# Optimization experiments

Hardware: AMD Instinct MI355X
Metric: run time of the kernel (lower is better)

The kernel has to match this reference:

```python
import jax, jax.numpy as jnp
import numpy as np

COMMITMENT_COST = 0.25  # pg_nn.VectorQuantizer default


def setup_inputs() -> dict:
    key = jax.random.key(0)
    k1, k2, k3, k4 = jax.random.split(key, 4)
    B, C, H, W = 32, 128, 64, 64
    D, K = 64, 512
    x = jax.random.normal(k1, (B, C, H, W), jnp.float32)
    # 1x1 conv == per-pixel linear projection; store weight as [D, C]
    conv_w = jax.random.normal(k2, (D, C), jnp.float32) * (1.0 / np.sqrt(C))
    conv_b = jax.random.normal(k3, (D,), jnp.float32) * 0.01
    # VectorQuantizer init: uniform(-1/K, 1/K)
    codebook = jax.random.uniform(k4, (K, D), jnp.float32, -1.0 / K, 1.0 / K)
    return {"x": x, "conv_w": conv_w, "conv_b": conv_b, "codebook": codebook}


def reference(x, conv_w, conv_b, codebook):
    # 1x1 conv projection: [B,C,H,W] -> [B,D,H,W]
    z = jnp.einsum('bchw,dc->bdhw', x, conv_w) + conv_b[None, :, None, None]
    B, D, H, W = z.shape
    flat = z.transpose(0, 2, 3, 1).reshape(-1, D)  # [B*H*W, D]
    # squared L2 distances to each codebook vector: [B*H*W, K]
    dists = (jnp.sum(flat * flat, axis=1, keepdims=True)
             - 2.0 * flat @ codebook.T
             + jnp.sum(codebook * codebook, axis=1))
    idx = jnp.argmin(dists, axis=1)  # [B*H*W]
    quantized = codebook[idx].reshape(B, H, W, D).transpose(0, 3, 1, 2)
    # VQ losses (commitment + embedding)
    commitment = COMMITMENT_COST * jnp.mean(jnp.square(jax.lax.stop_gradient(quantized) - z))
    emb_loss = jnp.mean(jnp.square(quantized - jax.lax.stop_gradient(z)))
    loss = commitment + emb_loss
    # straight-through estimator
    quantized_st = z + jax.lax.stop_gradient(quantized - z)
    return quantized_st, loss
```

## Files before the change

### kernel.cpp

```cpp
#include <hip/hip_runtime.h>
#include <hip/hip_bf16.h>
#include <math.h>

#define CIN   128
#define DDIM  64
#define KCB   512
#define HWSZ  4096
#define NPIX  131072
#define NOUTQ 8388608
#define XPAD  136

typedef short bf16x8 __attribute__((ext_vector_type(8)));
typedef float f32x4  __attribute__((ext_vector_type(4)));
typedef unsigned int u32x2 __attribute__((ext_vector_type(2)));

__device__ __forceinline__ unsigned int bcu(float f){ union{float f;unsigned int u;}v; v.f=f; return v.u; }
__device__ __forceinline__ float bcf(unsigned int u){ union{unsigned int u;float f;}v; v.u=u; return v.f; }
__device__ __forceinline__ unsigned int pkbf(float a, float b){
    union { __hip_bfloat162 h; unsigned int u; } v;
    v.h = __float22bfloat162_rn(make_float2(a, b));
    return v.u;
}

#define MFMA16(A, B, C) __builtin_amdgcn_mfma_f32_16x16x32_bf16((A), (B), (C), 0, 0, 0)

__device__ __forceinline__ void proj_tile(
    const float (&xr)[32], unsigned short* xrow,
    const unsigned short* sWA, const float* sBias,
    int lg, int klg, int l,
    f32x4& zA, f32x4& zB, f32x4& zC, f32x4& zD, bf16x8& zb0, bf16x8& zb1)
{
    #pragma unroll
    for (int j = 0; j < 8; ++j) {
        u32x2 pv = { pkbf(xr[4*j+0], xr[4*j+1]), pkbf(xr[4*j+2], xr[4*j+3]) };
        *(u32x2*)(xrow + lg * 32 + 4 * j) = pv;
    }
    zA = *(const f32x4*)(sBias +  0 + klg);
    zB = *(const f32x4*)(sBias + 16 + klg);
    zC = *(const f32x4*)(sBias + 32 + klg);
    zD = *(const f32x4*)(sBias + 48 + klg);
    #pragma unroll
    for (int ks = 0; ks < 4; ++ks) {
        bf16x8 xf = *(const bf16x8*)(xrow + ks * 32 + lg * 8);
        bf16x8 w0 = *(const bf16x8*)(sWA + ((0 * 4 + ks) * 64 + l) * 8);
        bf16x8 w1 = *(const bf16x8*)(sWA + ((1 * 4 + ks) * 64 + l) * 8);
        bf16x8 w2 = *(const bf16x8*)(sWA + ((2 * 4 + ks) * 64 + l) * 8);
        bf16x8 w3 = *(const bf16x8*)(sWA + ((3 * 4 + ks) * 64 + l) * 8);
        zA = MFMA16(w0, xf, zA);
        zB = MFMA16(w1, xf, zB);
        zC = MFMA16(w2, xf, zC);
        zD = MFMA16(w3, xf, zD);
    }
    unsigned int* zr = (unsigned int*)xrow;
    u32x2 z0 = { pkbf(zA[0], zA[1]), pkbf(zA[2], zA[3]) };
    u32x2 z1 = { pkbf(zB[0], zB[1]), pkbf(zB[2], zB[3]) };
    u32x2 z2 = { pkbf(zC[0], zC[1]), pkbf(zC[2], zC[3]) };
    u32x2 z3 = { pkbf(zD[0], zD[1]), pkbf(zD[2], zD[3]) };
    *(u32x2*)(zr +  0 + lg * 2) = z0;
    *(u32x2*)(zr +  8 + lg * 2) = z1;
    *(u32x2*)(zr + 16 + lg * 2) = z2;
    *(u32x2*)(zr + 24 + lg * 2) = z3;
    zb0 = *(const bf16x8*)(xrow + lg * 8);
    zb1 = *(const bf16x8*)(xrow + 32 + lg * 8);
}

__global__ __launch_bounds__(1024, 4) void vq_mfma(
    const float* __restrict__ x,
    const float* __restrict__ w,
    const float* __restrict__ bias,
    const float* __restrict__ cb,
    float* __restrict__ out,
    float* __restrict__ part)
{
    __shared__ __align__(16) unsigned short sCbA[KCB * DDIM];
    __shared__ __align__(16) unsigned short sWA[DDIM * CIN];
    __shared__ __align__(16) float sCbn[KCB];
    __shared__ __align__(16) float sBias[DDIM];
    __shared__ __align__(16) unsigned short sX[16 * 16 * XPAD];
    __shared__ float sLoss[16];

    const int t   = threadIdx.x;
    const int l   = t & 63;
    const int wv  = t >> 6;
    const int p16 = l & 15;
    const int lg  = l >> 4;
    const int klg = lg * 4;

    const int b   = blockIdx.x >> 3;
    const int hw0 = (blockIdx.x & 7) * 512 + wv * 32;
    const float* xp = x + ((size_t)b * CIN + (size_t)lg * 32) * HWSZ + hw0 + p16;
    float xr0[32], xr1[32];
    #pragma unroll
    for (int j = 0; j < 32; ++j) {
        xr0[j] = xp[(size_t)j * HWSZ];
        xr1[j] = xp[(size_t)j * HWSZ + 16];
    }

    #pragma unroll
    for (int it = 0; it < 8; ++it) {
        int i = t + it * 1024;
        int k = i >> 4, dg = i & 15;
        f32x4 v = *(const f32x4*)(cb + (size_t)k * DDIM + dg * 4);
        u32x2 pv = { pkbf(-2.f * v[0], -2.f * v[1]), pkbf(-2.f * v[2], -2.f * v[3]) };
        int ct = k >> 4, ks = dg >> 3, lhi = (dg >> 1) & 3, ll = (k & 15) | (lhi << 4);
        *(u32x2*)(sCbA + ((ct * 2 + ks) * 64 + ll) * 8 + (dg & 1) * 4) = pv;
    }
    #pragma unroll
    for (int it = 0; it < 2; ++it) {
        int i = t + it * 1024;
        int d = i >> 5, cg = i & 31;
        f32x4 v = *(const f32x4*)(w + (size_t)d * CIN + cg * 4);
        u32x2 pv = { pkbf(v[0], v[1]), pkbf(v[2], v[3]) };
        int dt = d >> 4, ks = cg >> 3, lhi = (cg >> 1) & 3, ll = (d & 15) | (lhi << 4);
        *(u32x2*)(sWA + ((dt * 4 + ks) * 64 + ll) * 8 + (cg & 1) * 4) = pv;
    }
    if (t < KCB) {
        const f32x4* row = (const f32x4*)(cb + (size_t)t * DDIM);
        float s = 0.f;
        #pragma unroll
        for (int j = 0; j < DDIM / 4; ++j) {
            f32x4 v = row[j];
            s = fmaf(v[0], v[0], s); s = fmaf(v[1], v[1], s);
            s = fmaf(v[2], v[2], s); s = fmaf(v[3], v[3], s);
        }
        sCbn[t] = s;
    }
    if (t < DDIM) sBias[t] = bias[t];
    __syncthreads();

    unsigned short* xrow = sX + wv * (16 * XPAD) + p16 * XPAD;

    f32x4 zaA0, zaA1, zaA2, zaA3, zaB0, zaB1, zaB2, zaB3;
    bf16x8 zb00, zb01, zb10, zb11;
    proj_tile(xr0, xrow, sWA, sBias, lg, klg, l, zaA0, zaA1, zaA2, zaA3, zb00, zb01);
    proj_tile(xr1, xrow, sWA, sBias, lg, klg, l, zaB0, zaB1, zaB2, zaB3, zb10, zb11);

    float rm00 = INFINITY, rm01 = INFINITY, rm10 = INFINITY, rm11 = INFINITY;
    #pragma unroll 4
    for (int ct = 0; ct < 32; ++ct) {
        f32x4 cinit = *(const f32x4*)(sCbn + ct * 16 + klg);
        bf16x8 c0 = *(const bf16x8*)(sCbA + ((ct * 2 + 0) * 64 + l) * 8);
        bf16x8 c1 = *(const bf16x8*)(sCbA + ((ct * 2 + 1) * 64 + l) * 8);
        f32x4 a0 = MFMA16(c0, zb00, cinit); a0 = MFMA16(c1, zb01, a0);
        f32x4 a1 = MFMA16(c0, zb10, cinit); a1 = MFMA16(c1, zb11, a1);
        unsigned int kb = (unsigned int)(ct * 16 + klg);
        rm00 = fminf(rm00, bcf((bcu(a0[0]) & 0xFFFFFE00u) | (kb + 0)));
        rm01 = fminf(rm01, bcf((bcu(a0[1]) & 0xFFFFFE00u) | (kb + 1)));
        rm00 = fminf(rm00, bcf((bcu(a0[2]) & 0xFFFFFE00u) | (kb + 2)));
        rm01 = fminf(rm01, bcf((bcu(a0[3]) & 0xFFFFFE00u) | (kb + 3)));
        rm10 = fminf(rm10, bcf((bcu(a1[0]) & 0xFFFFFE00u) | (kb + 0)));
        rm11 = fminf(rm11, bcf((bcu(a1[1]) & 0xFFFFFE00u) | (kb + 1)));
        rm10 = fminf(rm10, bcf((bcu(a1[2]) & 0xFFFFFE00u) | (kb + 2)));
        rm11 = fminf(rm11, bcf((bcu(a1[3]) & 0xFFFFFE00u) | (kb + 3)));
    }
    float rn0 = fminf(rm00, rm01);
    rn0 = fminf(rn0, __shfl_xor(rn0, 16, 64));
    rn0 = fminf(rn0, __shfl_xor(rn0, 32, 64));
    const int kbest0 = (int)(bcu(rn0) & 511u);
    float rn1 = fminf(rm10, rm11);
    rn1 = fminf(rn1, __shfl_xor(rn1, 16, 64));
    rn1 = fminf(rn1, __shfl_xor(rn1, 32, 64));
    const int kbest1 = (int)(bcu(rn1) & 511u);

    const float* q0r = cb + (size_t)kbest0 * DDIM;
    const float* q1r = cb + (size_t)kbest1 * DDIM;
    f32x4 qa0 = *(const f32x4*)(q0r +  0 + klg), qb0 = *(const f32x4*)(q1r +  0 + klg);
    f32x4 qa1 = *(const f32x4*)(q0r + 16 + klg), qb1 = *(const f32x4*)(q1r + 16 + klg);
    f32x4 qa2 = *(const f32x4*)(q0r + 32 + klg), qb2 = *(const f32x4*)(q1r + 32 + klg);
    f32x4 qa3 = *(const f32x4*)(q0r + 48 + klg), qb3 = *(const f32x4*)(q1r + 48 + klg);
    float lsum = 0.f;
    size_t ob = ((size_t)b * DDIM + klg) * (size_t)HWSZ + hw0 + p16;
    #pragma unroll
    for (int r = 0; r < 4; ++r) {
        float e;
        e = qa0[r] - zaA0[r]; lsum = fmaf(e, e, lsum);
        e = qb0[r] - zaB0[r]; lsum = fmaf(e, e, lsum);
        e = qa1[r] - zaA1[r]; lsum = fmaf(e, e, lsum);
        e = qb1[r] - zaB1[r]; lsum = fmaf(e, e, lsum);
        e = qa2[r] - zaA2[r]; lsum = fmaf(e, e, lsum);
        e = qb2[r] - zaB2[r]; lsum = fmaf(e, e, lsum);
        e = qa3[r] - zaA3[r]; lsum = fmaf(e, e, lsum);
        e = qb3[r] - zaB3[r]; lsum = fmaf(e, e, lsum);
        out[ob + (size_t)(r +  0) * HWSZ]      = qa0[r];
        out[ob + (size_t)(r +  0) * HWSZ + 16] = qb0[r];
        out[ob + (size_t)(r + 16) * HWSZ]      = qa1[r];
        out[ob + (size_t)(r + 16) * HWSZ + 16] = qb1[r];
        out[ob + (size_t)(r + 32) * HWSZ]      = qa2[r];
        out[ob + (size_t)(r + 32) * HWSZ + 16] = qb2[r];
        out[ob + (size_t)(r + 48) * HWSZ]      = qa3[r];
        out[ob + (size_t)(r + 48) * HWSZ + 16] = qb3[r];
    }

    #pragma unroll
    for (int off = 32; off > 0; off >>= 1)
        lsum += __shfl_down(lsum, off, 64);
    if (l == 0) sLoss[wv] = lsum;
    __syncthreads();
    if (wv == 0) {
        float v = (l < 16) ? sLoss[l] : 0.f;
        v += __shfl_down(v, 8, 64);
        v += __shfl_down(v, 4, 64);
        v += __shfl_down(v, 2, 64);
        v += __shfl_down(v, 1, 64);
        if (l == 0) part[blockIdx.x] = v;
    }
}

__global__ __launch_bounds__(256) void vq_loss(
    const float* __restrict__ part, float* __restrict__ loss_slot)
{
    __shared__ float sW[4];
    const int t = threadIdx.x;
    float s = part[t];
    #pragma unroll
    for (int off = 32; off > 0; off >>= 1) s += __shfl_down(s, off, 64);
    if ((t & 63) == 0) sW[t >> 6] = s;
    __syncthreads();
    if (t == 0)
        *loss_slot = (sW[0] + sW[1] + sW[2] + sW[3]) * (1.25f / (float)NOUTQ);
}

extern "C" void kernel_launch(void* const* d_in, const int* in_sizes, int n_in,
                              void* d_out, int out_size, void* d_ws, size_t ws_size,
                              hipStream_t stream) {
    const float* x    = (const float*)d_in[0];
    const float* w    = (const float*)d_in[1];
    const float* bias = (const float*)d_in[2];
    const float* cb   = (const float*)d_in[3];
    float* out = (float*)d_out;
    float* loss_slot = out + NOUTQ;
    float* part = (float*)d_ws;

    vq_mfma<<<256, 1024, 0, stream>>>(x, w, bias, cb, out, part);
    vq_loss<<<1,   256,  0, stream>>>(part, loss_slot);
}
```

Measured before the change: 40.57 us.

## Precompute codebook/weight fragments once in prep kernel, DMA into LDS

Adds a small prep kernel that converts the codebook and conv weight to bf16 MFMA fragment layout, computes codebook norms and copies the bias into a workspace blob. The main kernel then loads this blob straight into LDS with global_load_lds instead of having each of the 256 blocks redo the conversion and norm work. This removes redundant per-block ALU work and scattered LDS stores. In exchange it adds an extra kernel launch and a dependency between kernels.

```diff
diff --git a/kernel.cpp b/kernel.cpp
--- a/kernel.cpp
+++ b/kernel.cpp
@@ -6,13 +6,16 @@
 #define DDIM  64
 #define KCB   512
 #define HWSZ  4096
-#define NPIX  131072
 #define NOUTQ 8388608
 #define XPAD  136
 
 typedef short bf16x8 __attribute__((ext_vector_type(8)));
 typedef float f32x4  __attribute__((ext_vector_type(4)));
 typedef unsigned int u32x2 __attribute__((ext_vector_type(2)));
+
+#define BLOB_B   84992
+#define NCHUNK_B 83
+#define WS_PART  86016
 
 __device__ __forceinline__ unsigned int bcu(float f){ union{float f;unsigned int u;}v; v.f=f; return v.u; }
 __device__ __forceinline__ float bcf(unsigned int u){ union{unsigned int u;float f;}v; v.u=u; return v.f; }
@@ -23,6 +26,44 @@
 }
 
 #define MFMA16(A, B, C) __builtin_amdgcn_mfma_f32_16x16x32_bf16((A), (B), (C), 0, 0, 0)
+
+__global__ __launch_bounds__(256) void vq_prep(
+    const float* __restrict__ cb, const float* __restrict__ w,
+    const float* __restrict__ bias, unsigned char* __restrict__ blob)
+{
+    unsigned short* cbA = (unsigned short*)blob;
+    unsigned short* wA  = (unsigned short*)(blob + 65536);
+    float*          cbn = (float*)(blob + 81920);
+    float*          bia = (float*)(blob + 83968);
+
+    const int gid = blockIdx.x * 256 + threadIdx.x;
+    {
+        int k = gid >> 4, dg = gid & 15;
+        f32x4 v = *(const f32x4*)(cb + (size_t)k * DDIM + dg * 4);
+        u32x2 pv = { pkbf(-2.f * v[0], -2.f * v[1]), pkbf(-2.f * v[2], -2.f * v[3]) };
+        int ct = k >> 4, ks = dg >> 3, lhi = (dg >> 1) & 3, ll = (k & 15) | (lhi << 4);
+        *(u32x2*)(cbA + ((ct * 2 + ks) * 64 + ll) * 8 + (dg & 1) * 4) = pv;
+    }
+    if (gid < 2048) {
+        int d = gid >> 5, cg = gid & 31;
+        f32x4 v = *(const f32x4*)(w + (size_t)d * CIN + cg * 4);
+        u32x2 pv = { pkbf(v[0], v[1]), pkbf(v[2], v[3]) };
+        int dt = d >> 4, ks = cg >> 3, lhi = (cg >> 1) & 3, ll = (d & 15) | (lhi << 4);
+        *(u32x2*)(wA + ((dt * 4 + ks) * 64 + ll) * 8 + (cg & 1) * 4) = pv;
+    }
+    if (gid < KCB) {
+        const f32x4* row = (const f32x4*)(cb + (size_t)gid * DDIM);
+        float s = 0.f;
+        #pragma unroll
+        for (int j = 0; j < DDIM / 4; ++j) {
+            f32x4 v = row[j];
+            s = fmaf(v[0], v[0], s); s = fmaf(v[1], v[1], s);
+            s = fmaf(v[2], v[2], s); s = fmaf(v[3], v[3], s);
+        }
+        cbn[gid] = s;
+    }
+    if (gid < DDIM) bia[gid] = bias[gid];
+}
 
 __device__ __forceinline__ void proj_tile(
     const float (&xr)[32], unsigned short* xrow,
@@ -66,16 +107,12 @@
 
 __global__ __launch_bounds__(1024, 4) void vq_mfma(
     const float* __restrict__ x,
-    const float* __restrict__ w,
-    const float* __restrict__ bias,
     const float* __restrict__ cb,
+    const unsigned char* __restrict__ blob,
     float* __restrict__ out,
     float* __restrict__ part)
 {
-    __shared__ __align__(16) unsigned short sCbA[KCB * DDIM];
-    __shared__ __align__(16) unsigned short sWA[DDIM * CIN];
-    __shared__ __align__(16) float sCbn[KCB];
-    __shared__ __align__(16) float sBias[DDIM];
+    __shared__ __align__(16) unsigned char sFrag[BLOB_B];
     __shared__ __align__(16) unsigned short sX[16 * 16 * XPAD];
     __shared__ float sLoss[16];
 
@@ -86,6 +123,14 @@
     const int lg  = l >> 4;
     const int klg = lg * 4;
 
+    for (int i = wv; i < NCHUNK_B; i += 16) {
+        const unsigned char* g = blob + i * 1024 + l * 16;
+        unsigned char* s = sFrag + i * 1024;
+        __builtin_amdgcn_global_load_lds(
+            (const __attribute__((address_space(1))) unsigned int*)g,
+            (__attribute__((address_space(3))) unsigned int*)s, 16, 0, 0);
+    }
+
     const int b   = blockIdx.x >> 3;
     const int hw0 = (blockIdx.x & 7) * 512 + wv * 32;
     const float* xp = x + ((size_t)b * CIN + (size_t)lg * 32) * HWSZ + hw0 + p16;
@@ -95,38 +140,12 @@
         xr0[j] = xp[(size_t)j * HWSZ];
         xr1[j] = xp[(size_t)j * HWSZ + 16];
     }
-
-    #pragma unroll
-    for (int it = 0; it < 8; ++it) {
-        int i = t + it * 1024;
-        int k = i >> 4, dg = i & 15;
-        f32x4 v = *(const f32x4*)(cb + (size_t)k * DDIM + dg * 4);
-        u32x2 pv = { pkbf(-2.f * v[0], -2.f * v[1]), pkbf(-2.f * v[2], -2.f * v[3]) };
-        int ct = k >> 4, ks = dg >> 3, lhi = (dg >> 1) & 3, ll = (k & 15) | (lhi << 4);
-        *(u32x2*)(sCbA + ((ct * 2 + ks) * 64 + ll) * 8 + (dg & 1) * 4) = pv;
-    }
-    #pragma unroll
-    for (int it = 0; it < 2; ++it) {
-        int i = t + it * 1024;
-        int d = i >> 5, cg = i & 31;
-        f32x4 v = *(const f32x4*)(w + (size_t)d * CIN + cg * 4);
-        u32x2 pv = { pkbf(v[0], v[1]), pkbf(v[2], v[3]) };
-        int dt = d >> 4, ks = cg >> 3, lhi = (cg >> 1) & 3, ll = (d & 15) | (lhi << 4);
-        *(u32x2*)(sWA + ((dt * 4 + ks) * 64 + ll) * 8 + (cg & 1) * 4) = pv;
-    }
-    if (t < KCB) {
-        const f32x4* row = (const f32x4*)(cb + (size_t)t * DDIM);
-        float s = 0.f;
-        #pragma unroll
-        for (int j = 0; j < DDIM / 4; ++j) {
-            f32x4 v = row[j];
-            s = fmaf(v[0], v[0], s); s = fmaf(v[1], v[1], s);
-            s = fmaf(v[2], v[2], s); s = fmaf(v[3], v[3], s);
-        }
-        sCbn[t] = s;
-    }
-    if (t < DDIM) sBias[t] = bias[t];
     __syncthreads();
+
+    const unsigned short* sCbA = (const unsigned short*)sFrag;
+    const unsigned short* sWA  = (const unsigned short*)(sFrag + 65536);
+    const float*          sCbn = (const float*)(sFrag + 81920);
+    const float*          sBias= (const float*)(sFrag + 83968);
 
     unsigned short* xrow = sX + wv * (16 * XPAD) + p16 * XPAD;
 
@@ -229,8 +248,11 @@
     const float* cb   = (const float*)d_in[3];
     float* out = (float*)d_out;
     float* loss_slot = out + NOUTQ;
-    float* part = (float*)d_ws;
-
-    vq_mfma<<<256, 1024, 0, stream>>>(x, w, bias, cb, out, part);
+
+    unsigned char* blob = (unsigned char*)d_ws;
+    float* part = (float*)(blob + WS_PART);
+
+    vq_prep<<<32,  256,  0, stream>>>(cb, w, bias, blob);
+    vq_mfma<<<256, 1024, 0, stream>>>(x, cb, blob, out, part);
     vq_loss<<<1,   256,  0, stream>>>(part, loss_slot);
 }
```

After: 42.56 us. +4.9%, slower.
